# Kernel tuning notes

Hardware: AMD Instinct MI355X
Metric: run time of the kernel (lower is better)

Reference implementation:

```python
import jax, jax.numpy as jnp
import numpy as np

B, WIN, NN, F_IN, H = 8, 12, 2000, 8, 64
N = B * WIN * NN          # total graph nodes = 192000
E = 2_000_000             # edges
EPS = 1e-5                # BatchNorm eps
FC1_IN = 2 * H + WIN * F_IN + 1  # 225


def setup_inputs() -> dict:
    key = jax.random.key(0)
    ks = jax.random.split(key, 24)
    s = lambda k, shp: (jax.random.normal(k, shp, jnp.float32) * 0.05)
    d = {}
    d["adj_indices"] = jax.random.randint(ks[0], (2, E), 0, N)
    d["adj_weight"] = jax.random.uniform(ks[1], (E,), jnp.float32)
    d["x"] = jax.random.normal(ks[2], (N, F_IN), jnp.float32)
    d["inner_out"] = jax.random.normal(ks[3], (B * NN,), jnp.float32)
    # GCN layers
    d["W1"] = s(ks[4], (F_IN, H)); d["b1"] = jnp.zeros((H,), jnp.float32)
    d["W2"] = s(ks[5], (H, H));    d["b2"] = jnp.zeros((H,), jnp.float32)
    # BatchNorm affine params
    d["g1"] = jnp.ones((H,), jnp.float32);  d["be1"] = jnp.zeros((H,), jnp.float32)
    d["g2"] = jnp.ones((H,), jnp.float32);  d["be2"] = jnp.zeros((H,), jnp.float32)
    # LSTM 1 (input 2H) and LSTM 2 (input H); torch gate order i,f,g,o
    d["Wih1"] = s(ks[6], (4 * H, 2 * H)); d["Whh1"] = s(ks[7], (4 * H, H))
    d["bih1"] = jnp.zeros((4 * H,), jnp.float32); d["bhh1"] = jnp.zeros((4 * H,), jnp.float32)
    d["Wih2"] = s(ks[8], (4 * H, H)); d["Whh2"] = s(ks[9], (4 * H, H))
    d["bih2"] = jnp.zeros((4 * H,), jnp.float32); d["bhh2"] = jnp.zeros((4 * H,), jnp.float32)
    # FC head
    d["fc1_w"] = s(ks[10], (FC1_IN, H)); d["fc1_b"] = jnp.zeros((H,), jnp.float32)
    d["fc3_w"] = s(ks[11], (H, 1));      d["fc3_b"] = jnp.zeros((1,), jnp.float32)
    return d


def gcn(x, W, b, row, col, w):
    # PyG GCNConv: add self loops (weight 1), symmetric deg^-1/2 normalization,
    # aggregate messages from row (source) into col (target).
    loop = jnp.arange(N)
    r = jnp.concatenate([row, loop])
    c = jnp.concatenate([col, loop])
    ww = jnp.concatenate([w, jnp.ones((N,), w.dtype)])
    deg = jax.ops.segment_sum(ww, c, num_segments=N)
    dis = jnp.where(deg > 0, 1.0 / jnp.sqrt(deg), 0.0)
    norm = dis[r] * ww * dis[c]                      # [E+N]
    h = x @ W                                        # [N,H]
    out = jax.ops.segment_sum(h[r] * norm[:, None], c, num_segments=N)
    return out + b


def bn(x, g, b):  # training-mode BatchNorm1d (batch stats, biased var)
    m = x.mean(0)
    v = x.var(0)
    return (x - m) / jnp.sqrt(v + EPS) * g + b


def lstm(xs, Wih, Whh, bih, bhh):
    # xs: [T, Bn, D]; returns (all hidden states [T,Bn,H], last hidden [Bn,H])
    Bn = xs.shape[1]
    h0 = jnp.zeros((Bn, H), xs.dtype)
    def step(carry, xt):
        h, c = carry
        gates = xt @ Wih.T + h @ Whh.T + bih + bhh
        i, f, g, o = jnp.split(gates, 4, axis=-1)
        c = jax.nn.sigmoid(f) * c + jax.nn.sigmoid(i) * jnp.tanh(g)
        h = jax.nn.sigmoid(o) * jnp.tanh(c)
        return (h, c), h
    (hT, _), ys = jax.lax.scan(step, (h0, h0), xs)
    return ys, hT


def reference(adj_indices, adj_weight, x, inner_out,
              W1, b1, W2, b2, g1, be1, g2, be2,
              Wih1, Whh1, bih1, bhh1, Wih2, Whh2, bih2, bhh2,
              fc1_w, fc1_b, fc3_w, fc3_b):
    row, col = adj_indices[0], adj_indices[1]
    skip = x.reshape(B, WIN, NN, F_IN).transpose(0, 2, 1, 3).reshape(B * NN, WIN * F_IN)
    h1 = bn(jax.nn.relu(gcn(x, W1, b1, row, col, adj_weight)), g1, be1)   # dropout = identity (eval)
    h2 = bn(jax.nn.relu(gcn(h1, W2, b2, row, col, adj_weight)), g2, be2)
    h = jnp.concatenate([h1, h2], axis=1)                                  # [N, 2H]
    seq = h.reshape(B, WIN, NN, 2 * H).transpose(1, 0, 2, 3).reshape(WIN, B * NN, 2 * H)
    y1, hn1 = lstm(seq, Wih1, Whh1, bih1, bhh1)
    _, hn2 = lstm(y1, Wih2, Whh2, bih2, bhh2)
    z = jnp.concatenate([hn1, hn2, inner_out[:, None], skip], axis=1)      # [B*NN, FC1_IN]
    z = jax.nn.relu(z @ fc1_w + fc1_b)
    z = jax.nn.relu(z @ fc3_w + fc3_b)
    return z.reshape(-1)                                                   # [B*NN]
```

## Files before the change

kernel.cpp:

```cpp
#include <hip/hip_runtime.h>
#include <math.h>

#define N_NODES 192000
#define EDGES   2000000
#define HID     64
#define BN_ROWS 16000
#define T_WIN   12
#define B_SZ    8
#define NN_SZ   2000
#define FIN     8
#define BN_EPS  1e-5f

#define NBKT    750
#define NBLKA   1024
#define ACHUNK  1956
#define BKT_CAP 5120

typedef _Float16 f16x2 __attribute__((ext_vector_type(2)));
typedef _Float16 half4 __attribute__((ext_vector_type(4)));
typedef _Float16 half8 __attribute__((ext_vector_type(8)));
typedef float    f32x4 __attribute__((ext_vector_type(4)));
union F16x2U { float f; f16x2 h; };

__device__ __forceinline__ float frcp(float x){
#if __has_builtin(__builtin_amdgcn_rcpf)
    return __builtin_amdgcn_rcpf(x);
#else
    return 1.0f/x;
#endif
}
__device__ __forceinline__ float fsig(float x){ return frcp(1.0f + __expf(-x)); }
__device__ __forceinline__ float ftanh(float x){ return fmaf(2.0f, fsig(2.0f*x), -1.0f); }

__device__ __forceinline__ float packf16(float a, float b){
    F16x2U u; u.h[0] = (_Float16)a; u.h[1] = (_Float16)b; return u.f;
}

__global__ __launch_bounds__(256) void hist_coarse(
        const int* __restrict__ col, unsigned* __restrict__ gcount,
        int* __restrict__ blockbase){
    __shared__ unsigned bh[NBKT];
    int bl = blockIdx.x, tid = threadIdx.x;
    for (int i = tid; i < NBKT; i += 256) bh[i] = 0u;
    __syncthreads();
    int e0 = bl*ACHUNK;
    int e1 = e0 + ACHUNK; if (e1 > EDGES) e1 = EDGES;
    for (int e = e0 + tid*4; e < e1; e += 1024){
        int4 c4 = *(const int4*)&col[e];
        atomicAdd(&bh[((unsigned)c4.x) >> 8], 1u);
        atomicAdd(&bh[((unsigned)c4.y) >> 8], 1u);
        atomicAdd(&bh[((unsigned)c4.z) >> 8], 1u);
        atomicAdd(&bh[((unsigned)c4.w) >> 8], 1u);
    }
    __syncthreads();
    for (int i = tid; i < NBKT; i += 256)
        blockbase[bl*NBKT + i] = (int)atomicAdd(&gcount[i], bh[i]);
}

__global__ __launch_bounds__(1024) void scan_bkt(
        const unsigned* __restrict__ gcount, int* __restrict__ gbase,
        int* __restrict__ offsets){
    __shared__ int sm[1024];
    int tid = threadIdx.x;
    int v = (tid < NBKT) ? (int)gcount[tid] : 0;
    sm[tid] = v;
    __syncthreads();
    #pragma unroll
    for (int off = 1; off < 1024; off <<= 1){
        int t = (tid >= off) ? sm[tid - off] : 0;
        __syncthreads();
        sm[tid] += t;
        __syncthreads();
    }
    if (tid < NBKT) gbase[tid] = sm[tid] - v;
    if (tid == NBKT) gbase[NBKT] = EDGES;
    if (tid == NBKT+1) offsets[N_NODES] = EDGES;
}

__global__ __launch_bounds__(256) void scatter_bucket(
        const int* __restrict__ row, const int* __restrict__ col,
        const float* __restrict__ w, const int* __restrict__ blockbase,
        const int* __restrict__ gbase, int2* __restrict__ rec){
    __shared__ unsigned cur[NBKT];
    int bl = blockIdx.x, tid = threadIdx.x;
    for (int i = tid; i < NBKT; i += 256)
        cur[i] = (unsigned)(gbase[i] + blockbase[bl*NBKT + i]);
    __syncthreads();
    int e0 = bl*ACHUNK;
    int e1 = e0 + ACHUNK; if (e1 > EDGES) e1 = EDGES;
    for (int e = e0 + tid*4; e < e1; e += 1024){
        int4 r4 = *(const int4*)&row[e];
        int4 c4 = *(const int4*)&col[e];
        float4 w4 = *(const float4*)&w[e];
        int cc[4] = {c4.x, c4.y, c4.z, c4.w};
        int rr[4] = {r4.x, r4.y, r4.z, r4.w};
        float wf[4] = {w4.x, w4.y, w4.z, w4.w};
        #pragma unroll
        for (int q = 0; q < 4; q++){
            int c = cc[q];
            unsigned wfix = (unsigned)(wf[q]*16777216.0f + 0.5f);
            if (wfix > 0xFFFFFFu) wfix = 0xFFFFFFu;
            unsigned p = atomicAdd(&cur[((unsigned)c) >> 8], 1u);
            int2 rv; rv.x = rr[q];
            rv.y = (int)((((unsigned)(c & 255)) << 24) | wfix);
            rec[p] = rv;
        }
    }
}

__global__ __launch_bounds__(256) void bucket_csr(
        const int2* __restrict__ rec, const int* __restrict__ gbase,
        int2* __restrict__ edge_s, int* __restrict__ offsets,
        float* __restrict__ dis){
    __shared__ int2 S[BKT_CAP];
    __shared__ unsigned cnt[256];
    __shared__ unsigned wsum[256];
    __shared__ unsigned cur[256];
    __shared__ float dloc[256];
    int b = blockIdx.x, tid = threadIdx.x;
    int k0 = gbase[b], k1 = gbase[b+1];
    int n = k1 - k0;
    cnt[tid] = 0u; wsum[tid] = 0u;
    __syncthreads();
    bool staged = (n <= BKT_CAP);
    for (int i = tid; i < n; i += 256){
        int2 r = rec[k0 + i];
        if (staged) S[i] = r;
        unsigned clow = ((unsigned)r.y) >> 24;
        atomicAdd(&cnt[clow], 1u);
        atomicAdd(&wsum[clow], ((unsigned)r.y) & 0xFFFFFFu);
    }
    __syncthreads();
    unsigned v = cnt[tid];
    float deg = (float)wsum[tid] * (1.0f/16777216.0f);
    float dv = rsqrtf(deg + 1.0f);
    dloc[tid] = dv;
    dis[(b<<8) + tid] = dv;
    #pragma unroll
    for (int off = 1; off < 256; off <<= 1){
        unsigned t = (tid >= off) ? cnt[tid - off] : 0u;
        __syncthreads();
        cnt[tid] += t;
        __syncthreads();
    }
    unsigned excl = cnt[tid] - v;
    cur[tid] = excl;
    offsets[(b<<8) + tid] = k0 + (int)excl;
    __syncthreads();
    for (int i = tid; i < n; i += 256){
        int2 r = staged ? S[i] : rec[k0 + i];
        unsigned clow = ((unsigned)r.y) >> 24;
        unsigned wfix = ((unsigned)r.y) & 0xFFFFFFu;
        float sv = (float)wfix * (1.0f/16777216.0f) * dloc[clow];
        unsigned p = atomicAdd(&cur[clow], 1u);
        int2 o; o.x = r.x; o.y = __float_as_int(sv);
        edge_s[k0 + (int)p] = o;
    }
}

__global__ __launch_bounds__(256) void edge_fix(
        int2* __restrict__ edge_s, const float* __restrict__ dis){
    int i = blockIdx.x*256 + threadIdx.x;
    if (i >= EDGES) return;
    int2 e = edge_s[i];
    e.y = __float_as_int(dis[e.x]*__int_as_float(e.y));
    edge_s[i] = e;
}

__global__ __launch_bounds__(256) void aggx_bkt(
        const int2* __restrict__ rec, const int* __restrict__ gbase,
        const float* __restrict__ dis, const float* __restrict__ x,
        float* __restrict__ ax){
    __shared__ float acc[256*9];
    __shared__ float dloc[256];
    int b = blockIdx.x, tid = threadIdx.x;
    int gc = (b<<8) + tid;
    float dv = dis[gc];
    dloc[tid] = dv;
    float dd = dv*dv;
    float4 xa = *(const float4*)&x[(size_t)gc*8];
    float4 xb = *(const float4*)&x[(size_t)gc*8 + 4];
    acc[tid*9+0] = xa.x*dd; acc[tid*9+1] = xa.y*dd;
    acc[tid*9+2] = xa.z*dd; acc[tid*9+3] = xa.w*dd;
    acc[tid*9+4] = xb.x*dd; acc[tid*9+5] = xb.y*dd;
    acc[tid*9+6] = xb.z*dd; acc[tid*9+7] = xb.w*dd;
    __syncthreads();
    int k0 = gbase[b], k1 = gbase[b+1];
    int sub = tid & 7;
    for (int k = k0 + (tid >> 3); k < k1; k += 32){
        int2 r = rec[k];
        unsigned clow = ((unsigned)r.y) >> 24;
        float nw = (float)(((unsigned)r.y) & 0xFFFFFFu) * (1.0f/16777216.0f) * dloc[clow];
        float nr = dis[r.x] * nw;
        float xv = x[(size_t)r.x*8 + sub];
        atomicAdd(&acc[clow*9 + sub], xv*nr);
    }
    __syncthreads();
    float4 o0, o1;
    o0.x = acc[tid*9+0]; o0.y = acc[tid*9+1]; o0.z = acc[tid*9+2]; o0.w = acc[tid*9+3];
    o1.x = acc[tid*9+4]; o1.y = acc[tid*9+5]; o1.z = acc[tid*9+6]; o1.w = acc[tid*9+7];
    *(float4*)&ax[(size_t)gc*8]     = o0;
    *(float4*)&ax[(size_t)gc*8 + 4] = o1;
}

__global__ __launch_bounds__(256) void lin1b_stats(
        const float* __restrict__ ax, const float* __restrict__ W1,
        const float* __restrict__ b1, float* __restrict__ out,
        float* __restrict__ gsum, float* __restrict__ gsq){
    __shared__ float Ws[512];
    for (int i = threadIdx.x; i < 512; i += 256) Ws[i] = W1[i];
    __syncthreads();
    int f = threadIdx.x & 63;
    float wc[8];
    #pragma unroll
    for (int q = 0; q < 8; q++) wc[q] = Ws[q*64 + f];
    float bb = b1[f];
    float s = 0.f, s2 = 0.f;
    int stride = gridDim.x*blockDim.x;
    for (int idx = blockIdx.x*blockDim.x + threadIdx.x; idx < N_NODES*64; idx += stride){
        int j = idx >> 6;
        const float* ar = ax + (size_t)j*8;
        float acc = bb;
        #pragma unroll
        for (int q = 0; q < 8; q++) acc += ar[q]*wc[q];
        float v = fmaxf(acc, 0.f);
        out[idx] = v;
        s += v; s2 += v*v;
    }
    __shared__ float s1m[256], s2m[256];
    s1m[threadIdx.x] = s; s2m[threadIdx.x] = s2;
    __syncthreads();
    if (threadIdx.x < 64){
        float t1 = s1m[threadIdx.x]+s1m[threadIdx.x+64]+s1m[threadIdx.x+128]+s1m[threadIdx.x+192];
        float t2 = s2m[threadIdx.x]+s2m[threadIdx.x+64]+s2m[threadIdx.x+128]+s2m[threadIdx.x+192];
        atomicAdd(&gsum[threadIdx.x], t1);
        atomicAdd(&gsq[threadIdx.x], t2);
    }
}

#define L2ROWS 128
#define XS2    132
__global__ __launch_bounds__(128) void lin2_bn(
        const float* __restrict__ gcnA, const float* __restrict__ gsum,
        const float* __restrict__ gsq, const float* __restrict__ g1,
        const float* __restrict__ be1, const float* __restrict__ W2,
        _Float16* __restrict__ h1H, float* __restrict__ hlinH){
    __shared__ float Ws[64*64];
    __shared__ float xsT[64*XS2];
    int tid = threadIdx.x;
    int r0 = blockIdx.x * L2ROWS;

    for (int i = tid; i < 1024; i += 128)
        *(float4*)&Ws[i*4] = *(const float4*)&W2[i*4];

    int k4 = tid & 15;
    int rb = tid >> 4;
    float scv[4], shv[4];
    #pragma unroll
    for (int q = 0; q < 4; q++){
        int f = k4*4 + q;
        float mean = gsum[f]*(1.0f/(float)N_NODES);
        float var  = fmaxf(gsq[f]*(1.0f/(float)N_NODES) - mean*mean, 0.f);
        float sc_  = g1[f]*rsqrtf(var + BN_EPS);
        scv[q] = sc_; shv[q] = be1[f] - mean*sc_;
    }
    for (int it = 0; it < 16; it++){
        int r = it*8 + rb;
        float4 v = *(const float4*)&gcnA[(size_t)(r0+r)*64 + k4*4];
        v.x = v.x*scv[0]+shv[0]; v.y = v.y*scv[1]+shv[1];
        v.z = v.z*scv[2]+shv[2]; v.w = v.w*scv[3]+shv[3];
        half4 hh;
        hh[0]=(_Float16)v.x; hh[1]=(_Float16)v.y; hh[2]=(_Float16)v.z; hh[3]=(_Float16)v.w;
        *(half4*)&h1H[(size_t)(r0+r)*64 + k4*4] = hh;
        xsT[(k4*4+0)*XS2 + r] = v.x;
        xsT[(k4*4+1)*XS2 + r] = v.y;
        xsT[(k4*4+2)*XS2 + r] = v.z;
        xsT[(k4*4+3)*XS2 + r] = v.w;
    }
    __syncthreads();

    int cg = tid & 7;
    int rg = tid >> 3;
    float acc[8][8];
    #pragma unroll
    for (int i = 0; i < 8; i++)
        #pragma unroll
        for (int j = 0; j < 8; j++) acc[i][j] = 0.f;

    float4 a0 = *(float4*)&xsT[0*XS2 + rg*8];
    float4 a1 = *(float4*)&xsT[0*XS2 + rg*8 + 4];
    float4 w0 = *(float4*)&Ws[0*64 + cg*8];
    float4 w1 = *(float4*)&Ws[0*64 + cg*8 + 4];
    for (int k = 0; k < 64; k++){
        float4 na0, na1, nw0, nw1;
        if (k < 63){
            na0 = *(float4*)&xsT[(k+1)*XS2 + rg*8];
            na1 = *(float4*)&xsT[(k+1)*XS2 + rg*8 + 4];
            nw0 = *(float4*)&Ws[(k+1)*64 + cg*8];
            nw1 = *(float4*)&Ws[(k+1)*64 + cg*8 + 4];
        }
        float ar[8] = {a0.x,a0.y,a0.z,a0.w,a1.x,a1.y,a1.z,a1.w};
        float wcv[8] = {w0.x,w0.y,w0.z,w0.w,w1.x,w1.y,w1.z,w1.w};
        #pragma unroll
        for (int i = 0; i < 8; i++)
            #pragma unroll
            for (int j = 0; j < 8; j++) acc[i][j] += ar[i]*wcv[j];
        a0=na0; a1=na1; w0=nw0; w1=nw1;
    }
    #pragma unroll
    for (int i = 0; i < 8; i++){
        size_t r = (size_t)(r0 + rg*8 + i);
        float4 pk;
        pk.x = packf16(acc[i][0], acc[i][1]);
        pk.y = packf16(acc[i][2], acc[i][3]);
        pk.z = packf16(acc[i][4], acc[i][5]);
        pk.w = packf16(acc[i][6], acc[i][7]);
        *(float4*)&hlinH[r*32 + cg*4] = pk;
    }
}

__global__ __launch_bounds__(256) void gather2h(
        const int* __restrict__ offsets, const int2* __restrict__ edge_s,
        const float* __restrict__ dis, const float* __restrict__ hlinH,
        const float* __restrict__ bias, float* __restrict__ g2Hf){
    int j = blockIdx.x*8 + (threadIdx.x >> 5);
    int p = threadIdx.x & 31;
    float d = dis[j];
    float dd = d*d;
    F16x2U u; u.f = hlinH[(size_t)j*32 + p];
    float ax = (float)u.h[0]*dd;
    float ay = (float)u.h[1]*dd;
    int k  = offsets[j];
    int k1 = offsets[j+1];
    for (; k+4 <= k1; k += 4){
        int2 e0 = edge_s[k], e1 = edge_s[k+1], e2 = edge_s[k+2], e3 = edge_s[k+3];
        F16x2U a, b, c, e;
        a.f = hlinH[(size_t)e0.x*32 + p];
        b.f = hlinH[(size_t)e1.x*32 + p];
        c.f = hlinH[(size_t)e2.x*32 + p];
        e.f = hlinH[(size_t)e3.x*32 + p];
        float n0 = __int_as_float(e0.y), n1 = __int_as_float(e1.y);
        float n2 = __int_as_float(e2.y), n3 = __int_as_float(e3.y);
        ax += (float)a.h[0]*n0; ay += (float)a.h[1]*n0;
        ax += (float)b.h[0]*n1; ay += (float)b.h[1]*n1;
        ax += (float)c.h[0]*n2; ay += (float)c.h[1]*n2;
        ax += (float)e.h[0]*n3; ay += (float)e.h[1]*n3;
    }
    for (; k < k1; k++){
        int2 e0 = edge_s[k];
        F16x2U a; a.f = hlinH[(size_t)e0.x*32 + p];
        float n0 = __int_as_float(e0.y);
        ax += (float)a.h[0]*n0; ay += (float)a.h[1]*n0;
    }
    float2 bv = *(const float2*)&bias[2*p];
    float vx = fmaxf(ax + bv.x, 0.f);
    float vy = fmaxf(ay + bv.y, 0.f);
    F16x2U o; o.h[0] = (_Float16)vx; o.h[1] = (_Float16)vy;
    g2Hf[(size_t)j*32 + p] = o.f;
}

__global__ __launch_bounds__(256) void stats2h(
        const float* __restrict__ g2Hf, float* __restrict__ gsum2, float* __restrict__ gsq2){
    int p = threadIdx.x & 31;
    float s0 = 0.f, s1 = 0.f, q0 = 0.f, q1 = 0.f;
    int stride = gridDim.x*blockDim.x;
    for (int idx = blockIdx.x*blockDim.x + threadIdx.x; idx < N_NODES*32; idx += stride){
        F16x2U u; u.f = g2Hf[idx];
        float vx = (float)u.h[0], vy = (float)u.h[1];
        s0 += vx; q0 += vx*vx;
        s1 += vy; q1 += vy*vy;
    }
    __shared__ float sb[128];
    if (threadIdx.x < 128) sb[threadIdx.x] = 0.f;
    __syncthreads();
    atomicAdd(&sb[2*p],      s0);
    atomicAdd(&sb[2*p+1],    s1);
    atomicAdd(&sb[64+2*p],   q0);
    atomicAdd(&sb[64+2*p+1], q1);
    __syncthreads();
    if (threadIdx.x < 64){
        atomicAdd(&gsum2[threadIdx.x], sb[threadIdx.x]);
        atomicAdd(&gsq2[threadIdx.x],  sb[64+threadIdx.x]);
    }
}

__global__ void prep_weights(const float* __restrict__ Wih1, const float* __restrict__ Whh1,
                             const float* __restrict__ bih1, const float* __restrict__ bhh1,
                             const float* __restrict__ Wih2, const float* __restrict__ Whh2,
                             const float* __restrict__ bih2, const float* __restrict__ bhh2,
                             _Float16* W1F, _Float16* W2F, float* b1c, float* b2c){
    int idx = blockIdx.x*blockDim.x + threadIdx.x;
    if (idx < 6*256*32){
        int kt = idx >> 13;
        int rem = idx & 8191;
        int n = rem >> 5, kin = rem & 31;
        int k = kt*32 + kin;
        float v = (k < 128) ? Wih1[n*128 + k] : Whh1[n*64 + (k-128)];
        W1F[idx] = (_Float16)v;
    }
    int i2 = idx - 6*256*32;
    if (i2 >= 0 && i2 < 4*256*32){
        int kt = i2 >> 13;
        int rem = i2 & 8191;
        int n = rem >> 5, kin = rem & 31;
        int k = kt*32 + kin;
        float v = (k < 64) ? Wih2[n*64 + k] : Whh2[n*64 + (k-64)];
        W2F[i2] = (_Float16)v;
    }
    int i3 = idx - (6*256*32 + 4*256*32);
    if (i3 >= 0 && i3 < 256) b1c[i3] = bih1[i3] + bhh1[i3];
    int i4 = i3 - 256;
    if (i4 >= 0 && i4 < 256) b2c[i4] = bih2[i4] + bhh2[i4];
}

#define X1S 200
#define X2S 136
__global__ __launch_bounds__(256) void lstm_fused(
        const _Float16* __restrict__ h1H, const _Float16* __restrict__ g2H,
        const float* __restrict__ gsum2, const float* __restrict__ gsq2,
        const float* __restrict__ g2bn, const float* __restrict__ be2,
        const _Float16* __restrict__ W1F, const _Float16* __restrict__ W2F,
        const float* __restrict__ b1c, const float* __restrict__ b2c,
        float* __restrict__ h1s, float* __restrict__ h2s){
    __shared__ _Float16 X1h[16*X1S];
    __shared__ _Float16 X2h[16*X2S];
    int tid = threadIdx.x;
    int j0 = blockIdx.x*16;
    int w    = tid >> 6;
    int lane = tid & 63;
    int quad = lane >> 4;
    int l16  = lane & 15;
    int u    = 16*w + l16;

    int c4 = tid & 15;
    int sr = (tid >> 4) & 15;
    int sj = j0 + sr;
    int sb = sj / NN_SZ, sn = sj - sb*NN_SZ;
    size_t rbase = ((size_t)(sb*T_WIN)*NN_SZ + sn)*64 + c4*4;
    float sc2v[4], sh2v[4];
    #pragma unroll
    for (int q = 0; q < 4; q++){
        int f = c4*4 + q;
        float mean = gsum2[f]*(1.0f/(float)N_NODES);
        float var  = fmaxf(gsq2[f]*(1.0f/(float)N_NODES) - mean*mean, 0.f);
        float sc_  = g2bn[f]*rsqrtf(var + BN_EPS);
        sc2v[q] = sc_; sh2v[q] = be2[f] - mean*sc_;
    }

    float c1r[4], c2r[4], h2r[4];
    #pragma unroll
    for (int i = 0; i < 4; i++){ c1r[i] = 0.f; c2r[i] = 0.f; h2r[i] = 0.f; }

    float bi1 = b1c[u], bf1 = b1c[64+u], bg1 = b1c[128+u], bo1 = b1c[192+u];
    float bi2 = b2c[u], bf2 = b2c[64+u], bg2 = b2c[128+u], bo2 = b2c[192+u];

    {
        half4 v0 = *(const half4*)&h1H[rbase];
        half4 g4 = *(const half4*)&g2H[rbase];
        half4 v1;
        #pragma unroll
        for (int q = 0; q < 4; q++) v1[q] = (_Float16)((float)g4[q]*sc2v[q] + sh2v[q]);
        *(half4*)&X1h[sr*X1S + c4*4]       = v0;
        *(half4*)&X1h[sr*X1S + 64 + c4*4]  = v1;
        *(half4*)&X1h[sr*X1S + 128 + c4*4] = (half4){0,0,0,0};
    }
    __syncthreads();

    for (int t = 0; t < T_WIN; t++){
        half4 nv0, ng4;
        if (t < T_WIN-1){
            size_t rb = rbase + (size_t)(t+1)*NN_SZ*64;
            nv0 = *(const half4*)&h1H[rb];
            ng4 = *(const half4*)&g2H[rb];
        }

        f32x4 acc[4];
        #pragma unroll
        for (int g = 0; g < 4; g++) acc[g] = (f32x4){0.f,0.f,0.f,0.f};
        #pragma unroll
        for (int kt = 0; kt < 6; kt++){
            half8 a = *(const half8*)&X1h[l16*X1S + kt*32 + quad*8];
            #pragma unroll
            for (int g = 0; g < 4; g++){
                half8 b = *(const half8*)&W1F[(size_t)(kt*256 + 64*g + u)*32 + quad*8];
                acc[g] = __builtin_amdgcn_mfma_f32_16x16x32_f16(a, b, acc[g], 0, 0, 0);
            }
        }
        __syncthreads();

        #pragma unroll
        for (int r = 0; r < 4; r++){
            int rowl = quad*4 + r;
            float gi = acc[0][r] + bi1;
            float gf = acc[1][r] + bf1;
            float gg = acc[2][r] + bg1;
            float go = acc[3][r] + bo1;
            float cn = fsig(gf)*c1r[r] + fsig(gi)*ftanh(gg);
            float hn = fsig(go)*ftanh(cn);
            c1r[r] = cn;
            X2h[rowl*X2S + u]      = (_Float16)hn;
            X2h[rowl*X2S + 64 + u] = (_Float16)h2r[r];
            X1h[rowl*X1S + 128 + u] = (_Float16)hn;
            if (t == T_WIN-1) h1s[(size_t)(j0 + rowl)*64 + u] = hn;
        }
        if (t < T_WIN-1){
            half4 v1;
            #pragma unroll
            for (int q = 0; q < 4; q++) v1[q] = (_Float16)((float)ng4[q]*sc2v[q] + sh2v[q]);
            *(half4*)&X1h[sr*X1S + c4*4]      = nv0;
            *(half4*)&X1h[sr*X1S + 64 + c4*4] = v1;
        }
        __syncthreads();

        f32x4 acc2[4];
        #pragma unroll
        for (int g = 0; g < 4; g++) acc2[g] = (f32x4){0.f,0.f,0.f,0.f};
        #pragma unroll
        for (int kt = 0; kt < 4; kt++){
            half8 a = *(const half8*)&X2h[l16*X2S + kt*32 + quad*8];
            #pragma unroll
            for (int g = 0; g < 4; g++){
                half8 b = *(const half8*)&W2F[(size_t)(kt*256 + 64*g + u)*32 + quad*8];
                acc2[g] = __builtin_amdgcn_mfma_f32_16x16x32_f16(a, b, acc2[g], 0, 0, 0);
            }
        }

        #pragma unroll
        for (int r = 0; r < 4; r++){
            int rowl = quad*4 + r;
            float gi = acc2[0][r] + bi2;
            float gf = acc2[1][r] + bf2;
            float gg = acc2[2][r] + bg2;
            float go = acc2[3][r] + bo2;
            float cn = fsig(gf)*c2r[r] + fsig(gi)*ftanh(gg);
            float hn = fsig(go)*ftanh(cn);
            c2r[r] = cn;
            h2r[r] = hn;
            if (t == T_WIN-1) h2s[(size_t)(j0 + rowl)*64 + u] = hn;
        }
    }
}

__global__ __launch_bounds__(256) void fc_head(
        const float* __restrict__ h1s, const float* __restrict__ h2s,
        const float* __restrict__ inner, const float* __restrict__ x,
        const float* __restrict__ fc1_w, const float* __restrict__ fc1_b,
        const float* __restrict__ fc3_w, const float* __restrict__ fc3_b,
        float* __restrict__ out){
    __shared__ float zsm[4][226];
    int wv = threadIdx.x >> 6;
    int f  = threadIdx.x & 63;
    int j  = blockIdx.x*4 + wv;
    int b = j / NN_SZ, n = j - b*NN_SZ;
    for (int k = f; k < 225; k += 64){
        float v;
        if (k < 64)        v = h1s[j*64 + k];
        else if (k < 128)  v = h2s[j*64 + (k-64)];
        else if (k == 128) v = inner[j];
        else {
            int kk = k - 129;
            int w_ = kk >> 3, ff = kk & 7;
            v = x[((b*T_WIN + w_)*NN_SZ + n)*FIN + ff];
        }
        zsm[wv][k] = v;
    }
    __syncthreads();
    float acc = fc1_b[f];
    for (int k = 0; k < 225; k++) acc += zsm[wv][k]*fc1_w[k*64 + f];
    float p = fmaxf(acc, 0.f) * fc3_w[f];
    #pragma unroll
    for (int off = 32; off > 0; off >>= 1) p += __shfl_down(p, off, 64);
    if (f == 0) out[j] = fmaxf(p + fc3_b[0], 0.f);
}

extern "C" void kernel_launch(void* const* d_in, const int* in_sizes, int n_in,
                              void* d_out, int out_size, void* d_ws, size_t ws_size,
                              hipStream_t stream){
    const int*   adj  = (const int*)d_in[0];
    const int*   row  = adj;
    const int*   col  = adj + EDGES;
    const float* aw   = (const float*)d_in[1];
    const float* x    = (const float*)d_in[2];
    const float* inner= (const float*)d_in[3];
    const float* W1   = (const float*)d_in[4];
    const float* b1   = (const float*)d_in[5];
    const float* W2   = (const float*)d_in[6];
    const float* b2   = (const float*)d_in[7];
    const float* g1   = (const float*)d_in[8];
    const float* be1  = (const float*)d_in[9];
    const float* g2   = (const float*)d_in[10];
    const float* be2  = (const float*)d_in[11];
    const float* Wih1 = (const float*)d_in[12];
    const float* Whh1 = (const float*)d_in[13];
    const float* bih1 = (const float*)d_in[14];
    const float* bhh1 = (const float*)d_in[15];
    const float* Wih2 = (const float*)d_in[16];
    const float* Whh2 = (const float*)d_in[17];
    const float* bih2 = (const float*)d_in[18];
    const float* bhh2 = (const float*)d_in[19];
    const float* fc1w = (const float*)d_in[20];
    const float* fc1b = (const float*)d_in[21];
    const float* fc3w = (const float*)d_in[22];
    const float* fc3b = (const float*)d_in[23];
    float* out = (float*)d_out;

    float* ws = (float*)d_ws;
    const size_t NB = (size_t)N_NODES*64;
    float* bufX = ws;
    float* bufY = ws + NB;
    float* bufZ = ws + 2*NB;
    int2*  edge_s  = (int2*)(ws + 3*NB);
    float* degdis  = ws + 3*NB + (size_t)2*EDGES;
    float* gsum    = degdis + N_NODES;
    float* gsq     = gsum + 64;
    float* gsum2   = gsq + 64;
    float* gsq2    = gsum2 + 64;
    unsigned* gcount = (unsigned*)(gsq2 + 64);
    int* gbase   = (int*)(gcount + NBKT);
    int* offsets = gbase + (NBKT + 2);

    int* blockbase = (int*)bufX;
    int2* rec      = (int2*)bufY;

    float* hlinH = bufX;
    _Float16* h1H = (_Float16*)bufZ;
    float* ax    = bufZ + (size_t)N_NODES*32 + 64;
    float* gcnA1 = bufY;
    float* g2Hf  = bufY;

    float* h1s = bufX;
    float* h2s = bufX + (size_t)BN_ROWS*64;
    _Float16* W1F = (_Float16*)(bufX + (size_t)4*BN_ROWS*64);
    _Float16* W2F = W1F + 6*256*32;
    float* b1c = (float*)(W2F + 4*256*32);
    float* b2c = b1c + 256;

    hipMemsetAsync(gcount, 0, NBKT*sizeof(unsigned), stream);
    hipMemsetAsync(gsum, 0, 256*sizeof(float), stream);
    hist_coarse   <<<NBLKA, 256, 0, stream>>>(col, gcount, blockbase);
    scan_bkt      <<<1, 1024, 0, stream>>>(gcount, gbase, offsets);
    scatter_bucket<<<NBLKA, 256, 0, stream>>>(row, col, aw, blockbase, gbase, rec);
    bucket_csr    <<<NBKT, 256, 0, stream>>>(rec, gbase, edge_s, offsets, degdis);
    edge_fix      <<<(EDGES+255)/256, 256, 0, stream>>>(edge_s, degdis);

    aggx_bkt<<<NBKT, 256, 0, stream>>>(rec, gbase, degdis, x, ax);
    lin1b_stats<<<1024, 256, 0, stream>>>(ax, W1, b1, gcnA1, gsum, gsq);

    lin2_bn<<<N_NODES/L2ROWS, 128, 0, stream>>>(gcnA1, gsum, gsq, g1, be1, W2, h1H, hlinH);

    gather2h<<<N_NODES/8, 256, 0, stream>>>(offsets, edge_s, degdis, hlinH, b2, g2Hf);
    stats2h<<<1024, 256, 0, stream>>>(g2Hf, gsum2, gsq2);

    prep_weights<<<(6*256*32 + 4*256*32 + 512 + 255)/256, 256, 0, stream>>>(
        Wih1, Whh1, bih1, bhh1, Wih2, Whh2, bih2, bhh2, W1F, W2F, b1c, b2c);
    lstm_fused<<<BN_ROWS/16, 256, 0, stream>>>(h1H, (const _Float16*)g2Hf,
                                               gsum2, gsq2, g2, be2,
                                               W1F, W2F, b1c, b2c, h1s, h2s);

    fc_head<<<BN_ROWS/4, 256, 0, stream>>>(h1s, h2s, inner, x, fc1w, fc1b, fc3w, fc3b, out);
}
```

Before: 576.2 us.

## Aggregate layer-1 features from normalized CSR edges with two blocks per bucket

The bucket CSR records now pack the low 8 bits of the target column into the top byte of the source index, so the layer-1 feature aggregation can read the already-normalized edge_s array instead of re-deriving weights from the raw bucket records. Each bucket is split across two blocks that write separate partial sums, and these are added inside lin1b_stats. The edge loop is unrolled four ways for more memory-level parallelism. This removes per-edge dis lookups and weight decoding and doubles block-level parallelism, at the cost of an extra partial buffer read and masking in every consumer of edge_s.

Result: slower. 593.5 us (+3.0%).

```diff
diff --git a/kernel.cpp b/kernel.cpp
--- a/kernel.cpp
+++ b/kernel.cpp
@@ -153,7 +153,7 @@
         unsigned wfix = ((unsigned)r.y) & 0xFFFFFFu;
         float sv = (float)wfix * (1.0f/16777216.0f) * dloc[clow];
         unsigned p = atomicAdd(&cur[clow], 1u);
-        int2 o; o.x = r.x; o.y = __float_as_int(sv);
+        int2 o; o.x = (int)((clow << 24) | (unsigned)r.x); o.y = __float_as_int(sv);
         edge_s[k0 + (int)p] = o;
     }
 }
@@ -163,48 +163,66 @@
     int i = blockIdx.x*256 + threadIdx.x;
     if (i >= EDGES) return;
     int2 e = edge_s[i];
-    e.y = __float_as_int(dis[e.x]*__int_as_float(e.y));
+    e.y = __float_as_int(dis[e.x & 0xFFFFFF]*__int_as_float(e.y));
     edge_s[i] = e;
 }
 
-__global__ __launch_bounds__(256) void aggx_bkt(
-        const int2* __restrict__ rec, const int* __restrict__ gbase,
+__global__ __launch_bounds__(256) void aggx_es(
+        const int2* __restrict__ edge_s, const int* __restrict__ gbase,
         const float* __restrict__ dis, const float* __restrict__ x,
-        float* __restrict__ ax){
+        float* __restrict__ ax, float* __restrict__ ax2){
     __shared__ float acc[256*9];
-    __shared__ float dloc[256];
-    int b = blockIdx.x, tid = threadIdx.x;
+    int bb = blockIdx.x, tid = threadIdx.x;
+    int b = bb >> 1, part = bb & 1;
     int gc = (b<<8) + tid;
-    float dv = dis[gc];
-    dloc[tid] = dv;
-    float dd = dv*dv;
-    float4 xa = *(const float4*)&x[(size_t)gc*8];
-    float4 xb = *(const float4*)&x[(size_t)gc*8 + 4];
-    acc[tid*9+0] = xa.x*dd; acc[tid*9+1] = xa.y*dd;
-    acc[tid*9+2] = xa.z*dd; acc[tid*9+3] = xa.w*dd;
-    acc[tid*9+4] = xb.x*dd; acc[tid*9+5] = xb.y*dd;
-    acc[tid*9+6] = xb.z*dd; acc[tid*9+7] = xb.w*dd;
+    if (part == 0){
+        float dv = dis[gc];
+        float dd = dv*dv;
+        float4 xa = *(const float4*)&x[(size_t)gc*8];
+        float4 xb = *(const float4*)&x[(size_t)gc*8 + 4];
+        acc[tid*9+0] = xa.x*dd; acc[tid*9+1] = xa.y*dd;
+        acc[tid*9+2] = xa.z*dd; acc[tid*9+3] = xa.w*dd;
+        acc[tid*9+4] = xb.x*dd; acc[tid*9+5] = xb.y*dd;
+        acc[tid*9+6] = xb.z*dd; acc[tid*9+7] = xb.w*dd;
+    } else {
+        #pragma unroll
+        for (int q = 0; q < 8; q++) acc[tid*9+q] = 0.f;
+    }
     __syncthreads();
     int k0 = gbase[b], k1 = gbase[b+1];
     int sub = tid & 7;
-    for (int k = k0 + (tid >> 3); k < k1; k += 32){
-        int2 r = rec[k];
-        unsigned clow = ((unsigned)r.y) >> 24;
-        float nw = (float)(((unsigned)r.y) & 0xFFFFFFu) * (1.0f/16777216.0f) * dloc[clow];
-        float nr = dis[r.x] * nw;
-        float xv = x[(size_t)r.x*8 + sub];
-        atomicAdd(&acc[clow*9 + sub], xv*nr);
-    }
-    __syncthreads();
+    int k = k0 + part*32 + (tid >> 3);
+    for (; k + 192 < k1; k += 256){
+        int2 e0 = edge_s[k];
+        int2 e1 = edge_s[k+64];
+        int2 e2 = edge_s[k+128];
+        int2 e3 = edge_s[k+192];
+        float x0 = x[(size_t)(e0.x & 0xFFFFFF)*8 + sub];
+        float x1 = x[(size_t)(e1.x & 0xFFFFFF)*8 + sub];
+        float x2 = x[(size_t)(e2.x & 0xFFFFFF)*8 + sub];
+        float x3 = x[(size_t)(e3.x & 0xFFFFFF)*8 + sub];
+        atomicAdd(&acc[(((unsigned)e0.x) >> 24)*9 + sub], x0*__int_as_float(e0.y));
+        atomicAdd(&acc[(((unsigned)e1.x) >> 24)*9 + sub], x1*__int_as_float(e1.y));
+        atomicAdd(&acc[(((unsigned)e2.x) >> 24)*9 + sub], x2*__int_as_float(e2.y));
+        atomicAdd(&acc[(((unsigned)e3.x) >> 24)*9 + sub], x3*__int_as_float(e3.y));
+    }
+    for (; k < k1; k += 64){
+        int2 e0 = edge_s[k];
+        float x0 = x[(size_t)(e0.x & 0xFFFFFF)*8 + sub];
+        atomicAdd(&acc[(((unsigned)e0.x) >> 24)*9 + sub], x0*__int_as_float(e0.y));
+    }
+    __syncthreads();
+    float* dst = part ? ax2 : ax;
     float4 o0, o1;
     o0.x = acc[tid*9+0]; o0.y = acc[tid*9+1]; o0.z = acc[tid*9+2]; o0.w = acc[tid*9+3];
     o1.x = acc[tid*9+4]; o1.y = acc[tid*9+5]; o1.z = acc[tid*9+6]; o1.w = acc[tid*9+7];
-    *(float4*)&ax[(size_t)gc*8]     = o0;
-    *(float4*)&ax[(size_t)gc*8 + 4] = o1;
+    *(float4*)&dst[(size_t)gc*8]     = o0;
+    *(float4*)&dst[(size_t)gc*8 + 4] = o1;
 }
 
 __global__ __launch_bounds__(256) void lin1b_stats(
-        const float* __restrict__ ax, const float* __restrict__ W1,
+        const float* __restrict__ ax, const float* __restrict__ ax2,
+        const float* __restrict__ W1,
         const float* __restrict__ b1, float* __restrict__ out,
         float* __restrict__ gsum, float* __restrict__ gsq){
     __shared__ float Ws[512];
@@ -219,10 +237,11 @@
     int stride = gridDim.x*blockDim.x;
     for (int idx = blockIdx.x*blockDim.x + threadIdx.x; idx < N_NODES*64; idx += stride){
         int j = idx >> 6;
-        const float* ar = ax + (size_t)j*8;
+        const float* a1 = ax  + (size_t)j*8;
+        const float* a2 = ax2 + (size_t)j*8;
         float acc = bb;
         #pragma unroll
-        for (int q = 0; q < 8; q++) acc += ar[q]*wc[q];
+        for (int q = 0; q < 8; q++) acc += (a1[q]+a2[q])*wc[q];
         float v = fmaxf(acc, 0.f);
         out[idx] = v;
         s += v; s2 += v*v;
@@ -335,10 +354,10 @@
     for (; k+4 <= k1; k += 4){
         int2 e0 = edge_s[k], e1 = edge_s[k+1], e2 = edge_s[k+2], e3 = edge_s[k+3];
         F16x2U a, b, c, e;
-        a.f = hlinH[(size_t)e0.x*32 + p];
-        b.f = hlinH[(size_t)e1.x*32 + p];
-        c.f = hlinH[(size_t)e2.x*32 + p];
-        e.f = hlinH[(size_t)e3.x*32 + p];
+        a.f = hlinH[(size_t)(e0.x & 0xFFFFFF)*32 + p];
+        b.f = hlinH[(size_t)(e1.x & 0xFFFFFF)*32 + p];
+        c.f = hlinH[(size_t)(e2.x & 0xFFFFFF)*32 + p];
+        e.f = hlinH[(size_t)(e3.x & 0xFFFFFF)*32 + p];
         float n0 = __int_as_float(e0.y), n1 = __int_as_float(e1.y);
         float n2 = __int_as_float(e2.y), n3 = __int_as_float(e3.y);
         ax += (float)a.h[0]*n0; ay += (float)a.h[1]*n0;
@@ -348,7 +367,7 @@
     }
     for (; k < k1; k++){
         int2 e0 = edge_s[k];
-        F16x2U a; a.f = hlinH[(size_t)e0.x*32 + p];
+        F16x2U a; a.f = hlinH[(size_t)(e0.x & 0xFFFFFF)*32 + p];
         float n0 = __int_as_float(e0.y);
         ax += (float)a.h[0]*n0; ay += (float)a.h[1]*n0;
     }
@@ -621,6 +640,7 @@
 
     int* blockbase = (int*)bufX;
     int2* rec      = (int2*)bufY;
+    float* ax2     = bufX + 4*NBLKA*0 + (size_t)NBLKA*NBKT;
 
     float* hlinH = bufX;
     _Float16* h1H = (_Float16*)bufZ;
@@ -643,8 +663,8 @@
     bucket_csr    <<<NBKT, 256, 0, stream>>>(rec, gbase, edge_s, offsets, degdis);
     edge_fix      <<<(EDGES+255)/256, 256, 0, stream>>>(edge_s, degdis);
 
-    aggx_bkt<<<NBKT, 256, 0, stream>>>(rec, gbase, degdis, x, ax);
-    lin1b_stats<<<1024, 256, 0, stream>>>(ax, W1, b1, gcnA1, gsum, gsq);
+    aggx_es<<<NBKT*2, 256, 0, stream>>>(edge_s, gbase, degdis, x, ax, ax2);
+    lin1b_stats<<<1024, 256, 0, stream>>>(ax, ax2, W1, b1, gcnA1, gsum, gsq);
 
     lin2_bn<<<N_NODES/L2ROWS, 128, 0, stream>>>(gcnA1, gsum, gsq, g1, be1, W2, h1H, hlinH);
 
```
